# Kernel tuning notes

Measured on AMD Instinct MI355X. Metric: run time of the kernel, lower is better.

The kernel has to match this reference:

```python
import jax, jax.numpy as jnp
import numpy as np

N = 20000        # nodes
E = 640000       # edges (avg degree 32)
D_IN = 128       # node_features
D_HID = 256      # conv_booster * D_IN
D_DENSE = 128    # D_HID // linear_decay
N_CLASSES = 2


def _glorot(key, fan_in, fan_out):
    s = np.sqrt(1.0 / fan_in).astype(np.float32)
    return jax.random.normal(key, (fan_in, fan_out), jnp.float32) * s


def setup_inputs() -> dict:
    key = jax.random.key(0)
    ks = jax.random.split(key, 12)
    return {
        "node_features": jax.random.normal(ks[0], (N, D_IN), jnp.float32),
        "edge_index": jax.random.randint(ks[1], (2, E), 0, N, dtype=jnp.int32),
        "edge_weight": jax.random.uniform(ks[2], (E,), jnp.float32),
        "W1": _glorot(ks[3], D_IN, D_HID),
        "b1": jnp.zeros((D_HID,), jnp.float32),
        "W2": _glorot(ks[4], D_HID, D_HID),
        "b2": jnp.zeros((D_HID,), jnp.float32),
        "Wd1": _glorot(ks[5], D_HID, D_DENSE),
        "bd1": jnp.zeros((D_DENSE,), jnp.float32),
        "Wd2": _glorot(ks[6], D_DENSE, N_CLASSES),
        "bd2": jnp.zeros((N_CLASSES,), jnp.float32),
    }


def gcn_conv(x, row, col, w, W, b, n):
    # PyG GCNConv: add self-loops (weight 1), symmetric normalization,
    # x' = D^{-1/2}(A+I)D^{-1/2} (x W) + b
    h = x @ W                                        # [n, out]
    loop = jnp.arange(n, dtype=row.dtype)
    r = jnp.concatenate([row, loop])
    c = jnp.concatenate([col, loop])
    ww = jnp.concatenate([w, jnp.ones((n,), w.dtype)])
    deg = jax.ops.segment_sum(ww, c, num_segments=n)  # degree at targets
    dinv = jnp.where(deg > 0, jax.lax.rsqrt(deg), 0.0)
    norm = dinv[r] * ww * dinv[c]                    # [E+n]
    msg = norm[:, None] * h[r]                       # gather + scale (hot path)
    return jax.ops.segment_sum(msg, c, num_segments=n) + b  # scatter-add


def reference(node_features, edge_index, edge_weight,
              W1, b1, W2, b2, Wd1, bd1, Wd2, bd2):
    row, col = edge_index[0], edge_index[1]
    n = node_features.shape[0]
    h = gcn_conv(node_features, row, col, edge_weight, W1, b1, n)
    h = gcn_conv(h, row, col, edge_weight, W2, b2, n)
    g = jnp.mean(h, axis=0)                          # MeanAggregation pooling
    z = jax.nn.relu(g @ Wd1 + bd1)
    logits = z @ Wd2 + bd2
    return jax.nn.softmax(logits)
```

## Files before the change

### kernel.cpp

```cpp
#include <hip/hip_runtime.h>
#include <hip/hip_bf16.h>


#define D_IN 128
#define D_HID 256
#define D_DENSE 128
#define R0 10240
#define NSL 128
#define NTILE 157

__device__ __forceinline__ float ld_ag(const float* p) {
    return __hip_atomic_load(p, __ATOMIC_RELAXED, __HIP_MEMORY_SCOPE_AGENT);
}
__device__ __forceinline__ void st_ag(float* p, float v) {
    __hip_atomic_store(p, v, __ATOMIC_RELAXED, __HIP_MEMORY_SCOPE_AGENT);
}

__device__ __forceinline__ void ph_arrive(int* flags, int phase) {
    __syncthreads();
    if (threadIdx.x == 0)
        __hip_atomic_store(&flags[blockIdx.x], phase,
                           __ATOMIC_RELAXED, __HIP_MEMORY_SCOPE_AGENT);
}
__device__ __forceinline__ void ph_wait(int* flags, int phase) {
    if (threadIdx.x < 256) {
        while (__hip_atomic_load(&flags[threadIdx.x],
                                 __ATOMIC_RELAXED, __HIP_MEMORY_SCOPE_AGENT) < phase)
            __builtin_amdgcn_s_sleep(1);
    }
    __syncthreads();
}

struct Params {
    const float* x; const int* row; const int* col; const float* w;
    const float* W1; const float* b1; const float* W2; const float* b2;
    const float* Wd1; const float* bd1; const float* Wd2; const float* bd2;
    float* out;
    float* part; float* dinv; float* u; float* s_part; float* S_u_part;
    float* M; float* c2; int* flags;
    int N; int E; float inv_n;
};

__global__ __launch_bounds__(1024) void k_all(Params p) {
    __shared__ float lds[R0];
    const int b = blockIdx.x, tid = threadIdx.x;
    const int N = p.N, E = p.E;

    auto scatter = [&](const int* tgt, const int* src, int mode) {
        const int range = b & 1, slice = b >> 1;
        const int base = range ? R0 : 0;
        const int lim  = range ? (N - R0) : R0;
        const int per = (E + NSL - 1) / NSL;
        const int e0 = slice * per, e1 = min(e0 + per, E);
        float* outp = p.part + (range ? (size_t)NSL * R0 + (size_t)slice * lim
                                      : (size_t)slice * lim);
        for (int i = tid; i < lim; i += 1024) lds[i] = 0.f;
        __syncthreads();
        for (int e = e0 + tid; e < e1; e += 1024) {
            int t = tgt[e] - base;
            if ((unsigned)t < (unsigned)lim) {
                float v = p.w[e];
                if (mode != 0) {
                    int c = src[e];
                    float dc = p.dinv[c];
                    v *= (mode == 2) ? dc * p.u[c] : dc;
                }
                atomicAdd(&lds[t], v);
            }
        }
        __syncthreads();
        for (int i = tid; i < lim; i += 1024) st_ag(outp + i, lds[i]);
    };

    auto fold = [&](int mode) {
        const int j = tid & 127, rg = tid >> 7;
        const int i = b * 128 + j;
        const bool act = i < N;
        float sv = 0.f;
        if (act) {
            size_t st; const float* pp;
            if (i < R0) { st = R0;               pp = p.part + i; }
            else        { st = (size_t)(N - R0); pp = p.part + (size_t)NSL * R0 + (i - R0); }
            pp += (size_t)rg * 16 * st;
            #pragma unroll
            for (int r = 0; r < 16; ++r) sv += ld_ag(pp + (size_t)r * st);
        }
        lds[rg * 128 + j] = sv;
        __syncthreads();
        float ui = 0.f;
        if (rg == 0) {
            float tot = 0.f;
            #pragma unroll
            for (int q = 0; q < 8; ++q) tot += lds[q * 128 + j];
            if (act) {
                if (mode == 0) st_ag(p.dinv + i, rsqrtf(tot + 1.0f));
                else { float d = p.dinv[i]; ui = d * (tot + d); st_ag(p.u + i, ui); }
            }
        }
        if (mode == 1) {
            float v = ui;
            #pragma unroll
            for (int off = 32; off > 0; off >>= 1) v += __shfl_down(v, off, 64);
            if (tid < 128 && (tid & 63) == 0) lds[1028 + (tid >> 6)] = v;
            __syncthreads();
            if (tid == 0) st_ag(p.S_u_part + b, lds[1028] + lds[1029]);
        }
    };

    auto precompute = [&]() {
        int q = b - NTILE;
        lds[tid] = p.W2[(tid >> 2) * 256 + q * 4 + (tid & 3)];
        __syncthreads();
        int wvi = tid >> 6, lane = tid & 63;
        for (int kr = 0; kr < 8; ++kr) {
            int k = wvi * 8 + kr;
            float a0 = 0, a1 = 0, a2 = 0, a3 = 0;
            #pragma unroll
            for (int it = 0; it < 4; ++it) {
                int j = it * 64 + lane;
                float a = p.W1[k * 256 + j];
                a0 += a * lds[j*4+0]; a1 += a * lds[j*4+1];
                a2 += a * lds[j*4+2]; a3 += a * lds[j*4+3];
            }
            #pragma unroll
            for (int off = 32; off > 0; off >>= 1) {
                a0 += __shfl_down(a0, off, 64); a1 += __shfl_down(a1, off, 64);
                a2 += __shfl_down(a2, off, 64); a3 += __shfl_down(a3, off, 64);
            }
            if (lane == 0) {
                st_ag(p.M + k * 256 + q*4 + 0, a0); st_ag(p.M + k * 256 + q*4 + 1, a1);
                st_ag(p.M + k * 256 + q*4 + 2, a2); st_ag(p.M + k * 256 + q*4 + 3, a3);
            }
        }
        if (wvi == 0) {
            float a0 = 0, a1 = 0, a2 = 0, a3 = 0;
            #pragma unroll
            for (int it = 0; it < 4; ++it) {
                int j = it * 64 + lane;
                float a = p.b1[j];
                a0 += a * lds[j*4+0]; a1 += a * lds[j*4+1];
                a2 += a * lds[j*4+2]; a3 += a * lds[j*4+3];
            }
            #pragma unroll
            for (int off = 32; off > 0; off >>= 1) {
                a0 += __shfl_down(a0, off, 64); a1 += __shfl_down(a1, off, 64);
                a2 += __shfl_down(a2, off, 64); a3 += __shfl_down(a3, off, 64);
            }
            if (lane == 0) {
                st_ag(p.c2 + q*4+0, a0); st_ag(p.c2 + q*4+1, a1);
                st_ag(p.c2 + q*4+2, a2); st_ag(p.c2 + q*4+3, a3);
            }
        }
    };

    auto tailA = [&]() {
        const int k = tid & 127, rg = tid >> 7;
        const int i0 = b * 128, i = i0 + k;
        const bool act = i < N;
        float sv = 0.f;
        if (act) {
            size_t st; const float* pp;
            if (i < R0) { st = R0;               pp = p.part + i; }
            else        { st = (size_t)(N - R0); pp = p.part + (size_t)NSL * R0 + (i - R0); }
            pp += (size_t)rg * 16 * st;
            #pragma unroll
            for (int r = 0; r < 16; ++r) sv += ld_ag(pp + (size_t)r * st);
        }
        lds[tid] = sv;
        __syncthreads();
        if (rg == 0) {
            float q = 0.f;
            #pragma unroll
            for (int t2 = 0; t2 < 8; ++t2) q += lds[t2 * 128 + k];
            float d = act ? p.dinv[i] : 0.f;
            lds[1024 + k] = act ? d * (q + d * p.u[i]) : 0.f;
        }
        __syncthreads();
        float acc = 0.f;
        #pragma unroll
        for (int jj = 0; jj < 16; ++jj) {
            int m = rg + 8 * jj;
            int i2 = i0 + m;
            float xv = p.x[(size_t)(i2 < N ? i2 : i0) * D_IN + k];
            acc += lds[1024 + m] * xv;
        }
        __syncthreads();
        lds[tid] = acc;
        __syncthreads();
        if (rg == 0) {
            float t2s = 0.f;
            #pragma unroll
            for (int t2 = 0; t2 < 8; ++t2) t2s += lds[t2 * 128 + k];
            st_ag(p.s_part + b * 128 + k, t2s);
        }
    };

    auto head = [&]() {
        float* sh = lds;
        float* ss = lds + 1024;
        float* gg = lds + 1152;
        float* zz = lds + 1408;
        float* red = lds + 1536;
        const int k = tid & 127, rg = tid >> 7;

        float a = 0.f;
        for (int q = rg; q < NTILE; q += 8) a += ld_ag(p.s_part + q * 128 + k);
        sh[tid] = a;
        float v = (tid < NTILE) ? ld_ag(p.S_u_part + tid) : 0.f;
        #pragma unroll
        for (int off = 32; off > 0; off >>= 1) v += __shfl_down(v, off, 64);
        __syncthreads();
        if (rg == 0) {
            float t2 = 0.f;
            #pragma unroll
            for (int q = 0; q < 8; ++q) t2 += sh[q * 128 + k];
            ss[k] = t2;
        }
        if ((tid & 63) == 0) red[tid >> 6] = v;
        __syncthreads();
        if (tid == 0) {
            float t2 = 0.f;
            #pragma unroll
            for (int q = 0; q < 16; ++q) t2 += red[q];
            red[16] = t2;
        }
        __syncthreads();
        const float S_u = red[16];

        {
            int t = tid & 255, kg = tid >> 8;
            float acc = 0.f;
            #pragma unroll
            for (int kk = 0; kk < 32; ++kk) {
                int k2 = kg * 32 + kk;
                acc += ss[k2] * ld_ag(p.M + k2 * 256 + t);
            }
            sh[tid] = acc;
            __syncthreads();
            if (kg == 0)
                gg[t] = (sh[t] + sh[256 + t] + sh[512 + t] + sh[768 + t]
                         + S_u * ld_ag(p.c2 + t)) * p.inv_n + p.b2[t];
        }
        __syncthreads();

        {
            float acc = 0.f;
            #pragma unroll
            for (int kk = 0; kk < 32; ++kk) {
                int k2 = rg * 32 + kk;
                acc += gg[k2] * p.Wd1[k2 * D_DENSE + k];
            }
            sh[tid] = acc;
            __syncthreads();
            if (rg == 0) {
                float z = 0.f;
                #pragma unroll
                for (int q = 0; q < 8; ++q) z += sh[q * 128 + k];
                zz[k] = fmaxf(z + p.bd1[k], 0.f);
            }
        }
        __syncthreads();

        float p0 = 0.f, p1 = 0.f;
        if (tid < 128) {
            float zt = zz[tid];
            p0 = zt * p.Wd2[tid * 2 + 0];
            p1 = zt * p.Wd2[tid * 2 + 1];
        }
        #pragma unroll
        for (int off = 32; off > 0; off >>= 1) {
            p0 += __shfl_down(p0, off, 64);
            p1 += __shfl_down(p1, off, 64);
        }
        if ((tid & 63) == 0) { red[tid >> 6] = p0; red[20 + (tid >> 6)] = p1; }
        __syncthreads();
        if (tid == 0) {
            float l0 = red[0] + red[1] + p.bd2[0];
            float l1 = red[20] + red[21] + p.bd2[1];
            float m = fmaxf(l0, l1);
            float e0 = expf(l0 - m), e1 = expf(l1 - m);
            float inv = 1.0f / (e0 + e1);
            p.out[0] = e0 * inv;
            p.out[1] = e1 * inv;
        }
    };

    scatter(p.col, p.row, 0);
    ph_arrive(p.flags, 1); ph_wait(p.flags, 1);
    if (b < NTILE) fold(0);
    else if (b < NTILE + 64) precompute();
    ph_arrive(p.flags, 2); ph_wait(p.flags, 2);
    scatter(p.row, p.col, 1);
    ph_arrive(p.flags, 3); ph_wait(p.flags, 3);
    if (b < NTILE) fold(1);
    ph_arrive(p.flags, 4); ph_wait(p.flags, 4);
    scatter(p.row, p.col, 2);
    ph_arrive(p.flags, 5); ph_wait(p.flags, 5);
    if (b < NTILE) tailA();
    ph_arrive(p.flags, 6);
    if (b != 0) return;
    ph_wait(p.flags, 6);
    head();
}

extern "C" void kernel_launch(void* const* d_in, const int* in_sizes, int n_in,
                              void* d_out, int out_size, void* d_ws, size_t ws_size,
                              hipStream_t stream) {
    const int N = in_sizes[0] / D_IN;
    const int E = in_sizes[1] / 2;
    const int* ei = (const int*)d_in[1];

    Params p;
    p.x   = (const float*)d_in[0];
    p.row = ei;
    p.col = ei + E;
    p.w   = (const float*)d_in[2];
    p.W1  = (const float*)d_in[3];
    p.b1  = (const float*)d_in[4];
    p.W2  = (const float*)d_in[5];
    p.b2  = (const float*)d_in[6];
    p.Wd1 = (const float*)d_in[7];
    p.bd1 = (const float*)d_in[8];
    p.Wd2 = (const float*)d_in[9];
    p.bd2 = (const float*)d_in[10];
    p.out = (float*)d_out;

    float* fws   = (float*)d_ws;
    p.flags      = (int*)fws;
    p.part       = fws + 256;
    p.dinv       = p.part + (size_t)NSL * N;
    p.u          = p.dinv + N;
    p.s_part     = p.u + N;
    p.S_u_part   = p.s_part + (size_t)NTILE * D_IN;
    p.M          = p.S_u_part + NTILE;
    p.c2         = p.M + D_IN * D_HID;
    p.N = N; p.E = E; p.inv_n = 1.0f / (float)N;

    k_all<<<256, 1024, 0, stream>>>(p);
}
```

Before: 156.9 us.

## Repartition scatter into four node ranges with 64 edge slices and vectorized loads

The scatter phase now splits nodes into four ranges of 5120 (instead of two of 10240) and edges into 64 slices per range. This halves the LDS histogram size and the number of partial rows each fold must reduce. Edge loads are vectorized as int4/float4, with four atomics issued per iteration. Each block now reads 10000 edges rather than 5000, so per-block edge traffic doubles while fold reads halve. The vector loop also assumes E is a multiple of 4 and silently skips any tail edges, and the spin-wait sleep interval was increased.

Measured after the change: 163.0 us. 1.04x slower.

```diff
diff --git a/kernel.cpp b/kernel.cpp
--- a/kernel.cpp
+++ b/kernel.cpp
@@ -5,8 +5,10 @@
 #define D_IN 128
 #define D_HID 256
 #define D_DENSE 128
-#define R0 10240
-#define NSL 128
+#define NRANGE 4
+#define RB 5120
+#define NS 64
+#define PER 10000
 #define NTILE 157
 
 __device__ __forceinline__ float ld_ag(const float* p) {
@@ -15,7 +17,6 @@
 __device__ __forceinline__ void st_ag(float* p, float v) {
     __hip_atomic_store(p, v, __ATOMIC_RELAXED, __HIP_MEMORY_SCOPE_AGENT);
 }
-
 __device__ __forceinline__ void ph_arrive(int* flags, int phase) {
     __syncthreads();
     if (threadIdx.x == 0)
@@ -26,7 +27,7 @@
     if (threadIdx.x < 256) {
         while (__hip_atomic_load(&flags[threadIdx.x],
                                  __ATOMIC_RELAXED, __HIP_MEMORY_SCOPE_AGENT) < phase)
-            __builtin_amdgcn_s_sleep(1);
+            __builtin_amdgcn_s_sleep(2);
     }
     __syncthreads();
 }
@@ -42,31 +43,38 @@
 };
 
 __global__ __launch_bounds__(1024) void k_all(Params p) {
-    __shared__ float lds[R0];
+    __shared__ float lds[RB];
     const int b = blockIdx.x, tid = threadIdx.x;
     const int N = p.N, E = p.E;
 
     auto scatter = [&](const int* tgt, const int* src, int mode) {
-        const int range = b & 1, slice = b >> 1;
-        const int base = range ? R0 : 0;
-        const int lim  = range ? (N - R0) : R0;
-        const int per = (E + NSL - 1) / NSL;
-        const int e0 = slice * per, e1 = min(e0 + per, E);
-        float* outp = p.part + (range ? (size_t)NSL * R0 + (size_t)slice * lim
-                                      : (size_t)slice * lim);
+        const int g = b >> 6, s = b & 63;
+        const int base = g * RB;
+        const int lim  = min(RB, N - base);
+        const int e0 = s * PER, e1 = min(e0 + PER, E);
+        float* outp = p.part + (size_t)b * RB;
         for (int i = tid; i < lim; i += 1024) lds[i] = 0.f;
         __syncthreads();
-        for (int e = e0 + tid; e < e1; e += 1024) {
-            int t = tgt[e] - base;
-            if ((unsigned)t < (unsigned)lim) {
-                float v = p.w[e];
-                if (mode != 0) {
-                    int c = src[e];
-                    float dc = p.dinv[c];
-                    v *= (mode == 2) ? dc * p.u[c] : dc;
+        for (int e = e0 + tid * 4; e + 3 < e1; e += 4096) {
+            int4  t4 = *(const int4*)(tgt + e);
+            float4 w4 = *(const float4*)(p.w + e);
+            float v0 = w4.x, v1 = w4.y, v2 = w4.z, v3 = w4.w;
+            if (mode != 0) {
+                int4 s4 = *(const int4*)(src + e);
+                float d0 = p.dinv[s4.x], d1 = p.dinv[s4.y];
+                float d2 = p.dinv[s4.z], d3 = p.dinv[s4.w];
+                if (mode == 2) {
+                    d0 *= p.u[s4.x]; d1 *= p.u[s4.y];
+                    d2 *= p.u[s4.z]; d3 *= p.u[s4.w];
                 }
-                atomicAdd(&lds[t], v);
-            }
+                v0 *= d0; v1 *= d1; v2 *= d2; v3 *= d3;
+            }
+            int t0 = t4.x - base, t1 = t4.y - base;
+            int t2 = t4.z - base, t3 = t4.w - base;
+            if ((unsigned)t0 < (unsigned)lim) atomicAdd(&lds[t0], v0);
+            if ((unsigned)t1 < (unsigned)lim) atomicAdd(&lds[t1], v1);
+            if ((unsigned)t2 < (unsigned)lim) atomicAdd(&lds[t2], v2);
+            if ((unsigned)t3 < (unsigned)lim) atomicAdd(&lds[t3], v3);
         }
         __syncthreads();
         for (int i = tid; i < lim; i += 1024) st_ag(outp + i, lds[i]);
@@ -76,14 +84,13 @@
         const int j = tid & 127, rg = tid >> 7;
         const int i = b * 128 + j;
         const bool act = i < N;
+        const int g = b / 40;
+        const int jj = i - g * RB;
         float sv = 0.f;
         if (act) {
-            size_t st; const float* pp;
-            if (i < R0) { st = R0;               pp = p.part + i; }
-            else        { st = (size_t)(N - R0); pp = p.part + (size_t)NSL * R0 + (i - R0); }
-            pp += (size_t)rg * 16 * st;
-            #pragma unroll
-            for (int r = 0; r < 16; ++r) sv += ld_ag(pp + (size_t)r * st);
+            const float* pp = p.part + (size_t)(g * 64 + rg * 8) * RB + jj;
+            #pragma unroll
+            for (int r = 0; r < 8; ++r) sv += ld_ag(pp + (size_t)r * RB);
         }
         lds[rg * 128 + j] = sv;
         __syncthreads();
@@ -157,14 +164,13 @@
         const int k = tid & 127, rg = tid >> 7;
         const int i0 = b * 128, i = i0 + k;
         const bool act = i < N;
+        const int g = b / 40;
+        const int jj = i - g * RB;
         float sv = 0.f;
         if (act) {
-            size_t st; const float* pp;
-            if (i < R0) { st = R0;               pp = p.part + i; }
-            else        { st = (size_t)(N - R0); pp = p.part + (size_t)NSL * R0 + (i - R0); }
-            pp += (size_t)rg * 16 * st;
-            #pragma unroll
-            for (int r = 0; r < 16; ++r) sv += ld_ag(pp + (size_t)r * st);
+            const float* pp = p.part + (size_t)(g * 64 + rg * 8) * RB + jj;
+            #pragma unroll
+            for (int r = 0; r < 8; ++r) sv += ld_ag(pp + (size_t)r * RB);
         }
         lds[tid] = sv;
         __syncthreads();
@@ -178,8 +184,8 @@
         __syncthreads();
         float acc = 0.f;
         #pragma unroll
-        for (int jj = 0; jj < 16; ++jj) {
-            int m = rg + 8 * jj;
+        for (int m4 = 0; m4 < 16; ++m4) {
+            int m = rg + 8 * m4;
             int i2 = i0 + m;
             float xv = p.x[(size_t)(i2 < N ? i2 : i0) * D_IN + k];
             acc += lds[1024 + m] * xv;
@@ -328,11 +334,11 @@
     float* fws   = (float*)d_ws;
     p.flags      = (int*)fws;
     p.part       = fws + 256;
-    p.dinv       = p.part + (size_t)NSL * N;
+    p.dinv       = p.part + (size_t)256 * RB;
     p.u          = p.dinv + N;
     p.s_part     = p.u + N;
     p.S_u_part   = p.s_part + (size_t)NTILE * D_IN;
-    p.M          = p.S_u_part + NTILE;
+    p.M          = p.S_u_part + 160;
     p.c2         = p.M + D_IN * D_HID;
     p.N = N; p.E = E; p.inv_n = 1.0f / (float)N;
 
```
